# Performance work log

Measured on AMD Instinct MI355X. Metric: run time of the kernel, lower is better.

Reference implementation:

```python
import jax, jax.numpy as jnp
import numpy as np

N = 50000      # nodes
E = 512000     # directed edges (module assumes 2nd half is reverse of 1st half)
DIN = 128      # in_channels
EDIM = 128     # edge_dim (== in_channels, required by HypergraphConv branch)
H = 4          # heads
C = 32         # out_channels per head
EPS = 1e-5     # BatchNorm eps


def _segment_softmax(logits, seg, num):
    # PyG-style scatter softmax over segments (stable: subtract per-segment max)
    m = jax.ops.segment_max(logits, seg, num_segments=num)
    m = jnp.where(jnp.isfinite(m), m, 0.0)
    ex = jnp.exp(logits - m[seg])
    s = jax.ops.segment_sum(ex, seg, num_segments=num)
    return ex / (s[seg] + 1e-16)


def setup_inputs() -> dict:
    key = jax.random.key(0)
    ks = jax.random.split(key, 24)

    def lin(k, fin, fout):
        return (jax.random.normal(k, (fin, fout), jnp.float32) / np.sqrt(fin)).astype(jnp.float32)

    return {
        "x": jax.random.normal(ks[0], (N, DIN), jnp.float32),
        "edge_attr": jax.random.normal(ks[1], (E, EDIM), jnp.float32),
        # TransformerConv params
        "Wq": lin(ks[2], DIN, H * C), "bq": 0.01 * jax.random.normal(ks[3], (H * C,), jnp.float32),
        "Wk": lin(ks[4], DIN, H * C), "bk": 0.01 * jax.random.normal(ks[5], (H * C,), jnp.float32),
        "Wv": lin(ks[6], DIN, H * C), "bv": 0.01 * jax.random.normal(ks[7], (H * C,), jnp.float32),
        "We2": lin(ks[8], EDIM, H * C), "be2": 0.01 * jax.random.normal(ks[9], (H * C,), jnp.float32),
        "We3": lin(ks[10], EDIM, H * C), "be3": 0.01 * jax.random.normal(ks[11], (H * C,), jnp.float32),
        "Wcon": lin(ks[12], H * C, C),
        # BatchNorm1d params
        "bn_w": 1.0 + 0.01 * jax.random.normal(ks[13], (C,), jnp.float32),
        "bn_b": 0.01 * jax.random.normal(ks[14], (C,), jnp.float32),
        # HypergraphConv params (use_attention=False, heads=1)
        "Wh1": lin(ks[15], EDIM, C),
        "Wh2": lin(ks[16], DIN, C),
        "bh": jnp.zeros((C,), jnp.float32),
        # integer inputs
        "edge_index": jax.random.randint(ks[17], (2, E), 0, N, dtype=jnp.int32),
        "batch": jnp.zeros((N,), jnp.int32),
    }


def reference(x, edge_attr, Wq, bq, Wk, bk, Wv, bv, We2, be2, We3, be3, Wcon,
              bn_w, bn_b, Wh1, Wh2, bh, edge_index, batch):
    n = x.shape[0]
    e = edge_index.shape[1]
    src, dst = edge_index[0], edge_index[1]

    # ---- TransformerConv (edge-attention message passing) ----
    q = (x @ Wq + bq).reshape(n, H, C)
    k = (x @ Wk + bk).reshape(n, H, C)
    v = (x @ Wv + bv).reshape(n, H, C)
    ea2 = (edge_attr @ We2 + be2).reshape(e, H, C)
    ea3 = (edge_attr @ We3 + be3).reshape(e, H, C)
    qi, kj, vj = q[dst], k[src], v[src]          # gather per edge: [E,H,C]
    scale = 1.0 / np.sqrt(C)
    a1 = _segment_softmax((qi * kj).sum(-1) * scale, dst, n)    # [E,H]
    a2 = _segment_softmax((qi * ea2).sum(-1) * scale, dst, n)   # [E,H]
    msg = (vj * a1[..., None] + ea3 * a2[..., None]).reshape(e, H * C) @ Wcon  # [E,C]
    x_gat = jax.ops.segment_sum(msg, dst, num_segments=n)       # [N,C]

    # BatchNorm1d (training-mode batch stats, biased var) + exact GELU
    mu = x_gat.mean(0)
    var = ((x_gat - mu) ** 2).mean(0)
    x_gat = jax.nn.gelu(bn_w * (x_gat - mu) * jax.lax.rsqrt(var + EPS) + bn_b,
                        approximate=False)

    # ---- DHT dual hypergraph + HypergraphConv (no attention) ----
    e2 = e // 2
    ei = edge_index[:, :e2]           # first half of (bidirectional) edges
    ea = edge_attr[:e2]
    he_node = jnp.repeat(jnp.arange(e2, dtype=jnp.int32), 2)  # dual-node (edge) ids, [2*E2]
    he_edge = ei.T.reshape(-1)                                 # hyperedge (orig node) ids, [2*E2]

    xh = ea @ Wh1      # lin(edge_attr): [E2,C] (heads=1)
    attr = x @ Wh2     # lin2(x):        [N,C]

    ones = jnp.ones((2 * e2,), jnp.float32)
    deg_d = jax.ops.segment_sum(ones, he_node, num_segments=e2)   # D (== 2 per edge)
    Dinv = jnp.where(deg_d > 0, 1.0 / deg_d, 0.0)
    deg_b = jax.ops.segment_sum(ones, he_edge, num_segments=n)    # B (node degree)
    Binv = jnp.where(deg_b > 0, 1.0 / deg_b, 0.0)

    # propagate 1: dual-node -> hyperedge, norm B, then add hyperedge_attr
    o1 = jax.ops.segment_sum(Binv[he_edge][:, None] * xh[he_node],
                             he_edge, num_segments=n) + attr       # [N,C]
    # propagate 2 (flipped): hyperedge -> dual-node, norm D, add bias
    edge_attr2 = jax.ops.segment_sum(Dinv[he_node][:, None] * o1[he_edge],
                                     he_node, num_segments=e2) + bh  # [E2,C]

    return (x_gat, edge_attr2)
```

## Files before the change

kernel.cpp:

```cpp
#include <hip/hip_runtime.h>
#include <math.h>

#define NN 50000
#define NE 512000
#define NE2 256000
#define SCALE 0.17677669529663687f
#define EPSV 1e-5f
#define CHUNK 128000

#define OFF_Q      0UL
#define OFF_K      6400000UL
#define OFF_V      12800000UL
#define OFF_ATTR   0UL
#define OFF_O1     1600000UL
#define OFF_XGAT   3200000UL
#define OFF_O1ACC  4800000UL
#define OFF_DEGB   6400000UL
#define OFF_STATS  6450000UL
#define OFF_EX1    19200000UL
#define OFF_EX2    21248000UL
#define OFF_CC     23296000UL
#define OFF_S1     31488000UL
#define OFF_S2     31688000UL
#define OFF_XH     19200000UL
#define OFF_AGG    31888000UL
#define OFF_WBT    38288000UL
#define OFF_BIASB  38304384UL

typedef __attribute__((ext_vector_type(8))) short bf16x8;
typedef __attribute__((ext_vector_type(8))) unsigned short us8;
typedef __attribute__((ext_vector_type(4))) float f32x4;

__device__ __forceinline__ unsigned short f2bf(float f) {
    unsigned int u = __float_as_uint(f);
    unsigned int r = (u + 0x7FFFu + ((u >> 16) & 1u)) >> 16;
    return (unsigned short)r;
}
__device__ __forceinline__ float bf2f(unsigned short u) {
    return __uint_as_float(((unsigned int)u) << 16);
}

__global__ void pack_w(const float* __restrict__ We2, const float* __restrict__ be2,
                       const float* __restrict__ We3, const float* __restrict__ be3,
                       unsigned short* __restrict__ WbT, float* __restrict__ biasb) {
    const int idx = blockIdx.x * 256 + threadIdx.x;
    if (idx < 32768) {
        const int j = idx >> 7;
        const int k = idx & 127;
        const float w = (j < 128) ? We2[k * 128 + j] : We3[k * 128 + (j - 128)];
        WbT[idx] = f2bf(w);
    } else if (idx < 33024) {
        const int jj = idx - 32768;
        biasb[jj] = (jj < 128) ? be2[jj] : be3[jj - 128];
    }
}

__global__ __launch_bounds__(256)
void gemm_ea(const float* __restrict__ A, const unsigned short* __restrict__ WbT,
             const float* __restrict__ biasb, unsigned short* __restrict__ Cc, int half) {
    __shared__ unsigned short As[128 * 72];
    __shared__ unsigned short Bs[128 * 72];
    const int tid = threadIdx.x;
    const int wave = tid >> 6;
    const int lane = tid & 63;
    const int quad = lane >> 4;
    const int l16 = lane & 15;
    const int m0 = (wave & 1) * 64;
    const int n0 = (wave >> 1) * 64;
    const size_t r0 = (size_t)blockIdx.x * 128;

    f32x4 acc[4][4];
    #pragma unroll
    for (int i = 0; i < 4; i++)
        #pragma unroll
        for (int j = 0; j < 4; j++) acc[i][j] = (f32x4){0.f, 0.f, 0.f, 0.f};

    for (int kh = 0; kh < 2; kh++) {
        #pragma unroll
        for (int i = 0; i < 8; i++) {
            const int q = tid + 256 * i;
            const int row = q >> 4;
            const int c4 = q & 15;
            const float4 a4 = *(const float4*)(A + (r0 + row) * 128 + kh * 64 + c4 * 4);
            ushort4 b4;
            b4.x = f2bf(a4.x); b4.y = f2bf(a4.y); b4.z = f2bf(a4.z); b4.w = f2bf(a4.w);
            *(ushort4*)(&As[row * 72 + c4 * 4]) = b4;
        }
        {
            const int n = tid >> 1;
            const int koff = (tid & 1) * 32;
            const unsigned short* src = WbT + (size_t)(half * 128 + n) * 128 + kh * 64 + koff;
            #pragma unroll
            for (int u = 0; u < 4; u++) {
                *(us8*)(&Bs[n * 72 + koff + 8 * u]) = *(const us8*)(src + 8 * u);
            }
        }
        __syncthreads();
        #pragma unroll
        for (int kc = 0; kc < 64; kc += 32) {
            bf16x8 af[4], bf[4];
            #pragma unroll
            for (int i = 0; i < 4; i++)
                af[i] = *(const bf16x8*)(&As[(m0 + 16 * i + l16) * 72 + kc + quad * 8]);
            #pragma unroll
            for (int j = 0; j < 4; j++)
                bf[j] = *(const bf16x8*)(&Bs[(n0 + 16 * j + l16) * 72 + kc + quad * 8]);
            #pragma unroll
            for (int i = 0; i < 4; i++)
                #pragma unroll
                for (int j = 0; j < 4; j++)
                    acc[i][j] = __builtin_amdgcn_mfma_f32_16x16x32_bf16(af[i], bf[j], acc[i][j], 0, 0, 0);
        }
        __syncthreads();
    }
    #pragma unroll
    for (int j = 0; j < 4; j++) {
        const int col = n0 + 16 * j + l16;
        const float bcol = biasb[half * 128 + col];
        #pragma unroll
        for (int i = 0; i < 4; i++) {
            #pragma unroll
            for (int r = 0; r < 4; r++) {
                const int row = m0 + 16 * i + quad * 4 + r;
                Cc[(r0 + row) * 128 + col] = f2bf(acc[i][j][r] + bcol);
            }
        }
    }
}

__global__ void qkv_kernel(const float* __restrict__ x,
                           const float* __restrict__ Wq, const float* __restrict__ bq,
                           const float* __restrict__ Wk, const float* __restrict__ bk,
                           const float* __restrict__ Wv, const float* __restrict__ bv,
                           float* __restrict__ q, float* __restrict__ k, float* __restrict__ v) {
    __shared__ float xs[8 * 128];
    const int tid = threadIdx.x;
    const int j = tid & 127;
    const int g = tid >> 7;
    const size_t n0 = (size_t)blockIdx.x * 8;
    ((float4*)xs)[tid] = ((const float4*)(x + n0 * 128))[tid];
    __syncthreads();
    float aq[4] = {0,0,0,0}, ak[4] = {0,0,0,0}, av[4] = {0,0,0,0};
    #pragma unroll 4
    for (int d = 0; d < 128; d++) {
        const float wq = Wq[d*128 + j];
        const float wk = Wk[d*128 + j];
        const float wv = Wv[d*128 + j];
        #pragma unroll
        for (int r = 0; r < 4; r++) {
            const float xv = xs[(g + 2*r)*128 + d];
            aq[r] += xv * wq; ak[r] += xv * wk; av[r] += xv * wv;
        }
    }
    const float bqv = bq[j], bkv = bk[j], bvv = bv[j];
    #pragma unroll
    for (int r = 0; r < 4; r++) {
        const size_t n = n0 + g + 2*r;
        q[n*128 + j] = aq[r] + bqv;
        k[n*128 + j] = ak[r] + bkv;
        v[n*128 + j] = av[r] + bvv;
    }
}

__global__ void pass1(const int* __restrict__ eidx,
                      const float* __restrict__ q, const float* __restrict__ k,
                      const unsigned short* __restrict__ Cc, long e_base,
                      float* __restrict__ ex1, float* __restrict__ ex2,
                      float* __restrict__ s1, float* __restrict__ s2) {
    const size_t e = (size_t)e_base + blockIdx.x * 4 + (threadIdx.x >> 6);
    const int lane = threadIdx.x & 63;
    const int src = eidx[e];
    const int dst = eidx[NE + e];
    const float2 qv = ((const float2*)(q + (size_t)dst * 128))[lane];
    const float2 kv = ((const float2*)(k + (size_t)src * 128))[lane];
    const unsigned int cc = ((const unsigned int*)(Cc + (e - e_base) * 128))[lane];
    const float ea2a = bf2f((unsigned short)(cc & 0xFFFF));
    const float ea2b = bf2f((unsigned short)(cc >> 16));
    float p1 = qv.x * kv.x + qv.y * kv.y;
    float p2 = qv.x * ea2a + qv.y * ea2b;
    #pragma unroll
    for (int off = 8; off > 0; off >>= 1) {
        p1 += __shfl_down(p1, off, 16);
        p2 += __shfl_down(p2, off, 16);
    }
    if ((lane & 15) == 0) {
        const int h = lane >> 4;
        const float v1 = __expf(p1 * SCALE);
        const float v2 = __expf(p2 * SCALE);
        ex1[e * 4 + h] = v1;
        ex2[e * 4 + h] = v2;
        atomicAdd(&s1[(size_t)dst * 4 + h], v1);
        atomicAdd(&s2[(size_t)dst * 4 + h], v2);
    }
}

__global__ void pass2(const int* __restrict__ eidx,
                      const float* __restrict__ v,
                      const unsigned short* __restrict__ Cc, long e_base,
                      const float* __restrict__ ex1, const float* __restrict__ ex2,
                      const float* __restrict__ s1, const float* __restrict__ s2,
                      float* __restrict__ agg) {
    const size_t e = (size_t)e_base + blockIdx.x * 4 + (threadIdx.x >> 6);
    const int lane = threadIdx.x & 63;
    const int src = eidx[e];
    const int dst = eidx[NE + e];
    float a1l = 0.f, a2l = 0.f;
    if (lane < 4) {
        a1l = ex1[e * 4 + lane] / (s1[(size_t)dst * 4 + lane] + 1e-16f);
        a2l = ex2[e * 4 + lane] / (s2[(size_t)dst * 4 + lane] + 1e-16f);
    }
    const int h1 = lane >> 5;
    const int h2 = 2 + (lane >> 5);
    const float a1c1 = __shfl(a1l, h1), a1c2 = __shfl(a1l, h2);
    const float a2c1 = __shfl(a2l, h1), a2c2 = __shfl(a2l, h2);
    const float vv1 = v[(size_t)src * 128 + lane];
    const float vv2 = v[(size_t)src * 128 + lane + 64];
    const float e31 = bf2f(Cc[(e - e_base) * 128 + lane]);
    const float e32 = bf2f(Cc[(e - e_base) * 128 + lane + 64]);
    atomicAdd(&agg[(size_t)dst * 128 + lane],      a1c1 * vv1 + a2c1 * e31);
    atomicAdd(&agg[(size_t)dst * 128 + lane + 64], a1c2 * vv2 + a2c2 * e32);
}

__global__ void gemm_d128_o32(const float* __restrict__ A, const float* __restrict__ W,
                              float* __restrict__ out) {
    __shared__ float as[8 * 128];
    const int tid = threadIdx.x;
    const int p = tid & 31;
    const int mm = tid >> 5;
    const size_t m0 = (size_t)blockIdx.x * 8;
    ((float4*)as)[tid] = ((const float4*)(A + m0 * 128))[tid];
    __syncthreads();
    float c0 = 0.f, c1 = 0.f, c2 = 0.f, c3 = 0.f;
    const float4* as4 = (const float4*)as;
    #pragma unroll 8
    for (int i = 0; i < 32; i++) {
        const float4 a4 = as4[mm*32 + i];
        c0 += a4.x * W[(4*i+0)*32 + p];
        c1 += a4.y * W[(4*i+1)*32 + p];
        c2 += a4.z * W[(4*i+2)*32 + p];
        c3 += a4.w * W[(4*i+3)*32 + p];
    }
    out[(m0 + mm)*32 + p] = (c0 + c1) + (c2 + c3);
}

__global__ void bn_stats(const float* __restrict__ xg, float* __restrict__ stats) {
    __shared__ float ls[256], lss[256];
    const int tid = threadIdx.x;
    float s = 0.f, ss = 0.f;
    for (size_t i = (size_t)blockIdx.x*256 + tid; i < (size_t)NN*32; i += (size_t)gridDim.x*256) {
        const float val = xg[i];
        s += val; ss += val * val;
    }
    ls[tid] = s; lss[tid] = ss;
    __syncthreads();
    if (tid < 32) {
        float as_ = 0.f, ass = 0.f;
        #pragma unroll
        for (int w = 0; w < 8; w++) { as_ += ls[tid + 32*w]; ass += lss[tid + 32*w]; }
        atomicAdd(&stats[tid], as_);
        atomicAdd(&stats[32 + tid], ass);
    }
}

__global__ void bn_gelu(const float* __restrict__ xg, const float* __restrict__ stats,
                        const float* __restrict__ bnw, const float* __restrict__ bnb,
                        float* __restrict__ out) {
    const size_t i = (size_t)blockIdx.x * 256 + threadIdx.x;
    const int c = i & 31;
    const float mu = stats[c] * (1.0f / NN);
    const float var = stats[32 + c] * (1.0f / NN) - mu * mu;
    const float xn = bnw[c] * (xg[i] - mu) * rsqrtf(var + EPSV) + bnb[c];
    out[i] = 0.5f * xn * (1.0f + erff(xn * 0.70710678118654752f));
}

__global__ void hyper_scatter(const float* __restrict__ xh, const int* __restrict__ eidx,
                              float* __restrict__ o1acc, float* __restrict__ degb) {
    const int tid = threadIdx.x;
    const int c = tid & 31;
    const size_t i = (size_t)blockIdx.x * 8 + (tid >> 5);
    const int src = eidx[i];
    const int dst = eidx[NE + i];
    const float xv = xh[i*32 + c];
    atomicAdd(&o1acc[(size_t)src*32 + c], xv);
    atomicAdd(&o1acc[(size_t)dst*32 + c], xv);
    if (c == 0) {
        atomicAdd(&degb[src], 1.0f);
        atomicAdd(&degb[dst], 1.0f);
    }
}

__global__ void o1_finalize(const float* __restrict__ o1acc, const float* __restrict__ degb,
                            const float* __restrict__ attr, float* __restrict__ o1) {
    const size_t i = (size_t)blockIdx.x * 256 + threadIdx.x;
    const int n = (int)(i >> 5);
    const float d = degb[n];
    const float binv = d > 0.f ? 1.0f / d : 0.0f;
    o1[i] = o1acc[i] * binv + attr[i];
}

__global__ void edge_out(const float* __restrict__ o1, const int* __restrict__ eidx,
                         const float* __restrict__ bh, float* __restrict__ out2) {
    const size_t idx = (size_t)blockIdx.x * 256 + threadIdx.x;
    const size_t i = idx >> 5;
    const int c = (int)(idx & 31);
    const int src = eidx[i];
    const int dst = eidx[NE + i];
    out2[idx] = 0.5f * (o1[(size_t)src*32 + c] + o1[(size_t)dst*32 + c]) + bh[c];
}

extern "C" void kernel_launch(void* const* d_in, const int* in_sizes, int n_in,
                              void* d_out, int out_size, void* d_ws, size_t ws_size,
                              hipStream_t stream) {
    const float* x    = (const float*)d_in[0];
    const float* eatt = (const float*)d_in[1];
    const float* Wq   = (const float*)d_in[2];
    const float* bq   = (const float*)d_in[3];
    const float* Wk   = (const float*)d_in[4];
    const float* bk   = (const float*)d_in[5];
    const float* Wv   = (const float*)d_in[6];
    const float* bv   = (const float*)d_in[7];
    const float* We2  = (const float*)d_in[8];
    const float* be2  = (const float*)d_in[9];
    const float* We3  = (const float*)d_in[10];
    const float* be3  = (const float*)d_in[11];
    const float* Wcon = (const float*)d_in[12];
    const float* bnw  = (const float*)d_in[13];
    const float* bnb  = (const float*)d_in[14];
    const float* Wh1  = (const float*)d_in[15];
    const float* Wh2  = (const float*)d_in[16];
    const float* bh   = (const float*)d_in[17];
    const int*   eidx = (const int*)d_in[18];

    float* ws = (float*)d_ws;
    float* q     = ws + OFF_Q;
    float* k     = ws + OFF_K;
    float* v     = ws + OFF_V;
    float* ex1   = ws + OFF_EX1;
    float* ex2   = ws + OFF_EX2;
    unsigned short* Cc = (unsigned short*)(ws + OFF_CC);
    float* s1    = ws + OFF_S1;
    float* s2    = ws + OFF_S2;
    float* agg   = ws + OFF_AGG;
    unsigned short* WbT = (unsigned short*)(ws + OFF_WBT);
    float* biasb = ws + OFF_BIASB;
    float* attr  = ws + OFF_ATTR;
    float* o1    = ws + OFF_O1;
    float* xgat  = ws + OFF_XGAT;
    float* o1acc = ws + OFF_O1ACC;
    float* degb  = ws + OFF_DEGB;
    float* stats = ws + OFF_STATS;
    float* xh    = ws + OFF_XH;
    float* out0  = (float*)d_out;
    float* out1  = (float*)d_out + (size_t)NN * 32;

    hipMemsetAsync(ws + OFF_S1, 0, (38288000UL - OFF_S1) * sizeof(float), stream);

    pack_w<<<129, 256, 0, stream>>>(We2, be2, We3, be3, WbT, biasb);
    qkv_kernel<<<6250, 256, 0, stream>>>(x, Wq, bq, Wk, bk, Wv, bv, q, k, v);

    for (int c = 0; c < 4; c++) {
        const long eb = (long)c * CHUNK;
        gemm_ea<<<1000, 256, 0, stream>>>(eatt + (size_t)eb * 128, WbT, biasb, Cc, 0);
        pass1<<<32000, 256, 0, stream>>>(eidx, q, k, Cc, eb, ex1, ex2, s1, s2);
    }
    for (int c = 0; c < 4; c++) {
        const long eb = (long)c * CHUNK;
        gemm_ea<<<1000, 256, 0, stream>>>(eatt + (size_t)eb * 128, WbT, biasb, Cc, 1);
        pass2<<<32000, 256, 0, stream>>>(eidx, v, Cc, eb, ex1, ex2, s1, s2, agg);
    }

    hipMemsetAsync(ws + OFF_O1ACC, 0, (6450064UL - OFF_O1ACC) * sizeof(float), stream);

    gemm_d128_o32<<<6250, 256, 0, stream>>>(agg, Wcon, xgat);
    bn_stats<<<256, 256, 0, stream>>>(xgat, stats);
    bn_gelu<<<6250, 256, 0, stream>>>(xgat, stats, bnw, bnb, out0);

    gemm_d128_o32<<<32000, 256, 0, stream>>>(eatt, Wh1, xh);
    gemm_d128_o32<<<6250, 256, 0, stream>>>(x, Wh2, attr);
    hyper_scatter<<<32000, 256, 0, stream>>>(xh, eidx, o1acc, degb);
    o1_finalize<<<6250, 256, 0, stream>>>(o1acc, degb, attr, o1);
    edge_out<<<32000, 256, 0, stream>>>(o1, eidx, bh, out1);
}
```

Before: 1.294 ms.

## Fuse edge-attribute GEMM into attention passes via shared-memory staging

```diff
diff --git a/kernel.cpp b/kernel.cpp
--- a/kernel.cpp
+++ b/kernel.cpp
@@ -6,7 +6,6 @@
 #define NE2 256000
 #define SCALE 0.17677669529663687f
 #define EPSV 1e-5f
-#define CHUNK 128000
 
 #define OFF_Q      0UL
 #define OFF_K      6400000UL
@@ -19,7 +18,6 @@
 #define OFF_STATS  6450000UL
 #define OFF_EX1    19200000UL
 #define OFF_EX2    21248000UL
-#define OFF_CC     23296000UL
 #define OFF_S1     31488000UL
 #define OFF_S2     31688000UL
 #define OFF_XH     19200000UL
@@ -30,6 +28,8 @@
 typedef __attribute__((ext_vector_type(8))) short bf16x8;
 typedef __attribute__((ext_vector_type(8))) unsigned short us8;
 typedef __attribute__((ext_vector_type(4))) float f32x4;
+
+#define ESTRIDE 136
 
 __device__ __forceinline__ unsigned short f2bf(float f) {
     unsigned int u = __float_as_uint(f);
@@ -55,19 +55,18 @@
     }
 }
 
-__global__ __launch_bounds__(256)
-void gemm_ea(const float* __restrict__ A, const unsigned short* __restrict__ WbT,
-             const float* __restrict__ biasb, unsigned short* __restrict__ Cc, int half) {
-    __shared__ unsigned short As[128 * 72];
-    __shared__ unsigned short Bs[128 * 72];
-    const int tid = threadIdx.x;
+__device__ __forceinline__ void gemm_tile(const float* __restrict__ A,
+                                          const unsigned short* __restrict__ WbT,
+                                          const float* __restrict__ biasb, const int half,
+                                          unsigned short* sh, const size_t r0, const int tid) {
+    unsigned short* As = sh;
+    unsigned short* Bs = sh + 9216;
     const int wave = tid >> 6;
     const int lane = tid & 63;
     const int quad = lane >> 4;
     const int l16 = lane & 15;
     const int m0 = (wave & 1) * 64;
     const int n0 = (wave >> 1) * 64;
-    const size_t r0 = (size_t)blockIdx.x * 128;
 
     f32x4 acc[4][4];
     #pragma unroll
@@ -122,9 +121,89 @@
             #pragma unroll
             for (int r = 0; r < 4; r++) {
                 const int row = m0 + 16 * i + quad * 4 + r;
-                Cc[(r0 + row) * 128 + col] = f2bf(acc[i][j][r] + bcol);
+                sh[row * ESTRIDE + col] = f2bf(acc[i][j][r] + bcol);
             }
         }
+    }
+    __syncthreads();
+}
+
+__global__ __launch_bounds__(256)
+void gemm_pass1(const float* __restrict__ eatt, const unsigned short* __restrict__ WbT,
+                const float* __restrict__ biasb, const int* __restrict__ eidx,
+                const float* __restrict__ q, const float* __restrict__ k,
+                float* __restrict__ ex1, float* __restrict__ ex2,
+                float* __restrict__ s1, float* __restrict__ s2) {
+    __shared__ unsigned short sh[18432];
+    const int tid = threadIdx.x;
+    const size_t r0 = (size_t)blockIdx.x * 128;
+    gemm_tile(eatt, WbT, biasb, 0, sh, r0, tid);
+
+    const int wave = tid >> 6;
+    const int lane = tid & 63;
+    for (int t = 0; t < 32; t++) {
+        const int lrow = wave * 32 + t;
+        const size_t e = r0 + lrow;
+        const int src = eidx[e];
+        const int dst = eidx[NE + e];
+        const float2 qv = ((const float2*)(q + (size_t)dst * 128))[lane];
+        const float2 kv = ((const float2*)(k + (size_t)src * 128))[lane];
+        const unsigned int cc = *(const unsigned int*)(&sh[lrow * ESTRIDE + lane * 2]);
+        const float ea2a = bf2f((unsigned short)(cc & 0xFFFF));
+        const float ea2b = bf2f((unsigned short)(cc >> 16));
+        float p1 = qv.x * kv.x + qv.y * kv.y;
+        float p2 = qv.x * ea2a + qv.y * ea2b;
+        #pragma unroll
+        for (int off = 8; off > 0; off >>= 1) {
+            p1 += __shfl_down(p1, off, 16);
+            p2 += __shfl_down(p2, off, 16);
+        }
+        if ((lane & 15) == 0) {
+            const int h = lane >> 4;
+            const float v1 = __expf(p1 * SCALE);
+            const float v2 = __expf(p2 * SCALE);
+            ex1[e * 4 + h] = v1;
+            ex2[e * 4 + h] = v2;
+            atomicAdd(&s1[(size_t)dst * 4 + h], v1);
+            atomicAdd(&s2[(size_t)dst * 4 + h], v2);
+        }
+    }
+}
+
+__global__ __launch_bounds__(256)
+void gemm_pass2(const float* __restrict__ eatt, const unsigned short* __restrict__ WbT,
+                const float* __restrict__ biasb, const int* __restrict__ eidx,
+                const float* __restrict__ v,
+                const float* __restrict__ ex1, const float* __restrict__ ex2,
+                const float* __restrict__ s1, const float* __restrict__ s2,
+                float* __restrict__ agg) {
+    __shared__ unsigned short sh[18432];
+    const int tid = threadIdx.x;
+    const size_t r0 = (size_t)blockIdx.x * 128;
+    gemm_tile(eatt, WbT, biasb, 1, sh, r0, tid);
+
+    const int wave = tid >> 6;
+    const int lane = tid & 63;
+    for (int t = 0; t < 32; t++) {
+        const int lrow = wave * 32 + t;
+        const size_t e = r0 + lrow;
+        const int src = eidx[e];
+        const int dst = eidx[NE + e];
+        float a1l = 0.f, a2l = 0.f;
+        if (lane < 4) {
+            a1l = ex1[e * 4 + lane] / (s1[(size_t)dst * 4 + lane] + 1e-16f);
+            a2l = ex2[e * 4 + lane] / (s2[(size_t)dst * 4 + lane] + 1e-16f);
+        }
+        const int h1 = lane >> 5;
+        const int h2 = 2 + (lane >> 5);
+        const float a1c1 = __shfl(a1l, h1), a1c2 = __shfl(a1l, h2);
+        const float a2c1 = __shfl(a2l, h1), a2c2 = __shfl(a2l, h2);
+        const float vv1 = v[(size_t)src * 128 + lane];
+        const float vv2 = v[(size_t)src * 128 + lane + 64];
+        const float e31 = bf2f(sh[lrow * ESTRIDE + lane]);
+        const float e32 = bf2f(sh[lrow * ESTRIDE + lane + 64]);
+        atomicAdd(&agg[(size_t)dst * 128 + lane],      a1c1 * vv1 + a2c1 * e31);
+        atomicAdd(&agg[(size_t)dst * 128 + lane + 64], a1c2 * vv2 + a2c2 * e32);
     }
 }
 
@@ -160,65 +239,6 @@
         k[n*128 + j] = ak[r] + bkv;
         v[n*128 + j] = av[r] + bvv;
     }
-}
-
-__global__ void pass1(const int* __restrict__ eidx,
-                      const float* __restrict__ q, const float* __restrict__ k,
-                      const unsigned short* __restrict__ Cc, long e_base,
-                      float* __restrict__ ex1, float* __restrict__ ex2,
-                      float* __restrict__ s1, float* __restrict__ s2) {
-    const size_t e = (size_t)e_base + blockIdx.x * 4 + (threadIdx.x >> 6);
-    const int lane = threadIdx.x & 63;
-    const int src = eidx[e];
-    const int dst = eidx[NE + e];
-    const float2 qv = ((const float2*)(q + (size_t)dst * 128))[lane];
-    const float2 kv = ((const float2*)(k + (size_t)src * 128))[lane];
-    const unsigned int cc = ((const unsigned int*)(Cc + (e - e_base) * 128))[lane];
-    const float ea2a = bf2f((unsigned short)(cc & 0xFFFF));
-    const float ea2b = bf2f((unsigned short)(cc >> 16));
-    float p1 = qv.x * kv.x + qv.y * kv.y;
-    float p2 = qv.x * ea2a + qv.y * ea2b;
-    #pragma unroll
-    for (int off = 8; off > 0; off >>= 1) {
-        p1 += __shfl_down(p1, off, 16);
-        p2 += __shfl_down(p2, off, 16);
-    }
-    if ((lane & 15) == 0) {
-        const int h = lane >> 4;
-        const float v1 = __expf(p1 * SCALE);
-        const float v2 = __expf(p2 * SCALE);
-        ex1[e * 4 + h] = v1;
-        ex2[e * 4 + h] = v2;
-        atomicAdd(&s1[(size_t)dst * 4 + h], v1);
-        atomicAdd(&s2[(size_t)dst * 4 + h], v2);
-    }
-}
-
-__global__ void pass2(const int* __restrict__ eidx,
-                      const float* __restrict__ v,
-                      const unsigned short* __restrict__ Cc, long e_base,
-                      const float* __restrict__ ex1, const float* __restrict__ ex2,
-                      const float* __restrict__ s1, const float* __restrict__ s2,
-                      float* __restrict__ agg) {
-    const size_t e = (size_t)e_base + blockIdx.x * 4 + (threadIdx.x >> 6);
-    const int lane = threadIdx.x & 63;
-    const int src = eidx[e];
-    const int dst = eidx[NE + e];
-    float a1l = 0.f, a2l = 0.f;
-    if (lane < 4) {
-        a1l = ex1[e * 4 + lane] / (s1[(size_t)dst * 4 + lane] + 1e-16f);
-        a2l = ex2[e * 4 + lane] / (s2[(size_t)dst * 4 + lane] + 1e-16f);
-    }
-    const int h1 = lane >> 5;
-    const int h2 = 2 + (lane >> 5);
-    const float a1c1 = __shfl(a1l, h1), a1c2 = __shfl(a1l, h2);
-    const float a2c1 = __shfl(a2l, h1), a2c2 = __shfl(a2l, h2);
-    const float vv1 = v[(size_t)src * 128 + lane];
-    const float vv2 = v[(size_t)src * 128 + lane + 64];
-    const float e31 = bf2f(Cc[(e - e_base) * 128 + lane]);
-    const float e32 = bf2f(Cc[(e - e_base) * 128 + lane + 64]);
-    atomicAdd(&agg[(size_t)dst * 128 + lane],      a1c1 * vv1 + a2c1 * e31);
-    atomicAdd(&agg[(size_t)dst * 128 + lane + 64], a1c2 * vv2 + a2c2 * e32);
 }
 
 __global__ void gemm_d128_o32(const float* __restrict__ A, const float* __restrict__ W,
@@ -337,7 +357,6 @@
     float* v     = ws + OFF_V;
     float* ex1   = ws + OFF_EX1;
     float* ex2   = ws + OFF_EX2;
-    unsigned short* Cc = (unsigned short*)(ws + OFF_CC);
     float* s1    = ws + OFF_S1;
     float* s2    = ws + OFF_S2;
     float* agg   = ws + OFF_AGG;
@@ -358,16 +377,8 @@
     pack_w<<<129, 256, 0, stream>>>(We2, be2, We3, be3, WbT, biasb);
     qkv_kernel<<<6250, 256, 0, stream>>>(x, Wq, bq, Wk, bk, Wv, bv, q, k, v);
 
-    for (int c = 0; c < 4; c++) {
-        const long eb = (long)c * CHUNK;
-        gemm_ea<<<1000, 256, 0, stream>>>(eatt + (size_t)eb * 128, WbT, biasb, Cc, 0);
-        pass1<<<32000, 256, 0, stream>>>(eidx, q, k, Cc, eb, ex1, ex2, s1, s2);
-    }
-    for (int c = 0; c < 4; c++) {
-        const long eb = (long)c * CHUNK;
-        gemm_ea<<<1000, 256, 0, stream>>>(eatt + (size_t)eb * 128, WbT, biasb, Cc, 1);
-        pass2<<<32000, 256, 0, stream>>>(eidx, v, Cc, eb, ex1, ex2, s1, s2, agg);
-    }
+    gemm_pass1<<<4000, 256, 0, stream>>>(eatt, WbT, biasb, eidx, q, k, ex1, ex2, s1, s2);
+    gemm_pass2<<<4000, 256, 0, stream>>>(eatt, WbT, biasb, eidx, v, ex1, ex2, s1, s2, agg);
 
     hipMemsetAsync(ws + OFF_O1ACC, 0, (6450064UL - OFF_O1ACC) * sizeof(float), stream);
 
```

Result: slower. 1.404 ms (+8.5%).

## Sort edges by destination (CSR) and fuse attention passes without atomics

Applied to the files above, without the earlier changes.

```diff
diff --git a/kernel.cpp b/kernel.cpp
--- a/kernel.cpp
+++ b/kernel.cpp
@@ -6,7 +6,6 @@
 #define NE2 256000
 #define SCALE 0.17677669529663687f
 #define EPSV 1e-5f
-#define CHUNK 128000
 
 #define OFF_Q      0UL
 #define OFF_K      6400000UL
@@ -19,13 +18,18 @@
 #define OFF_STATS  6450000UL
 #define OFF_EX1    19200000UL
 #define OFF_EX2    21248000UL
-#define OFF_CC     23296000UL
-#define OFF_S1     31488000UL
-#define OFF_S2     31688000UL
 #define OFF_XH     19200000UL
-#define OFF_AGG    31888000UL
-#define OFF_WBT    38288000UL
-#define OFF_BIASB  38304384UL
+#define OFF_CC2    23296000UL
+#define OFF_CC3    56064000UL
+#define OFF_SEG    88832000UL
+#define OFF_CUR    88883000UL
+#define OFF_CNT    88933000UL
+#define OFF_INV    88983000UL
+#define OFF_SRCS   89495000UL
+#define OFF_PART   90007000UL
+#define OFF_WBT    90008000UL
+#define OFF_BIASB  90024384UL
+#define OFF_AGG    90024640UL
 
 typedef __attribute__((ext_vector_type(8))) short bf16x8;
 typedef __attribute__((ext_vector_type(8))) unsigned short us8;
@@ -55,9 +59,64 @@
     }
 }
 
+__global__ void k_hist(const int* __restrict__ eidx, int* __restrict__ cnt) {
+    const int e = blockIdx.x * 256 + threadIdx.x;
+    atomicAdd(&cnt[eidx[NE + e]], 1);
+}
+
+__global__ void k_scanA(const int* __restrict__ cnt, int* __restrict__ seg,
+                        int* __restrict__ part) {
+    __shared__ int sd[256];
+    const int tid = threadIdx.x;
+    const int i = blockIdx.x * 256 + tid;
+    const int v = (i < NN) ? cnt[i] : 0;
+    sd[tid] = v;
+    __syncthreads();
+    for (int off = 1; off < 256; off <<= 1) {
+        int t = (tid >= off) ? sd[tid - off] : 0;
+        __syncthreads();
+        sd[tid] += t;
+        __syncthreads();
+    }
+    if (i < NN) seg[i] = sd[tid] - v;
+    if (tid == 255) part[blockIdx.x] = sd[255];
+}
+
+__global__ void k_scanB(int* __restrict__ part) {
+    __shared__ int sd[256];
+    const int tid = threadIdx.x;
+    const int v = (tid < 196) ? part[tid] : 0;
+    sd[tid] = v;
+    __syncthreads();
+    for (int off = 1; off < 256; off <<= 1) {
+        int t = (tid >= off) ? sd[tid - off] : 0;
+        __syncthreads();
+        sd[tid] += t;
+        __syncthreads();
+    }
+    if (tid < 196) part[tid] = sd[tid] - v;
+}
+
+__global__ void k_scanC(int* __restrict__ seg, const int* __restrict__ part) {
+    const int i = blockIdx.x * 256 + threadIdx.x;
+    if (i < NN) seg[i] += part[blockIdx.x];
+    if (i == 0) seg[NN] = NE;
+}
+
+__global__ void k_scatter(const int* __restrict__ eidx, const int* __restrict__ seg,
+                          int* __restrict__ cur, int* __restrict__ inv,
+                          int* __restrict__ srcs) {
+    const int e = blockIdx.x * 256 + threadIdx.x;
+    const int dst = eidx[NE + e];
+    const int pos = seg[dst] + atomicAdd(&cur[dst], 1);
+    inv[e] = pos;
+    srcs[pos] = eidx[e];
+}
+
 __global__ __launch_bounds__(256)
 void gemm_ea(const float* __restrict__ A, const unsigned short* __restrict__ WbT,
-             const float* __restrict__ biasb, unsigned short* __restrict__ Cc, int half) {
+             const float* __restrict__ biasb, const int* __restrict__ inv,
+             unsigned short* __restrict__ Cc, int half) {
     __shared__ unsigned short As[128 * 72];
     __shared__ unsigned short Bs[128 * 72];
     const int tid = threadIdx.x;
@@ -113,6 +172,12 @@
         }
         __syncthreads();
     }
+    int posr[16];
+    #pragma unroll
+    for (int i = 0; i < 4; i++)
+        #pragma unroll
+        for (int r = 0; r < 4; r++)
+            posr[i * 4 + r] = inv[r0 + m0 + 16 * i + quad * 4 + r];
     #pragma unroll
     for (int j = 0; j < 4; j++) {
         const int col = n0 + 16 * j + l16;
@@ -121,8 +186,7 @@
         for (int i = 0; i < 4; i++) {
             #pragma unroll
             for (int r = 0; r < 4; r++) {
-                const int row = m0 + 16 * i + quad * 4 + r;
-                Cc[(r0 + row) * 128 + col] = f2bf(acc[i][j][r] + bcol);
+                Cc[(size_t)posr[i * 4 + r] * 128 + col] = f2bf(acc[i][j][r] + bcol);
             }
         }
     }
@@ -162,63 +226,56 @@
     }
 }
 
-__global__ void pass1(const int* __restrict__ eidx,
-                      const float* __restrict__ q, const float* __restrict__ k,
-                      const unsigned short* __restrict__ Cc, long e_base,
-                      float* __restrict__ ex1, float* __restrict__ ex2,
-                      float* __restrict__ s1, float* __restrict__ s2) {
-    const size_t e = (size_t)e_base + blockIdx.x * 4 + (threadIdx.x >> 6);
+__global__ __launch_bounds__(256)
+void attn_pass(const int* __restrict__ seg, const int* __restrict__ srcs,
+               const float* __restrict__ q, const float* __restrict__ k,
+               const float* __restrict__ v,
+               const unsigned short* __restrict__ Cc2, const unsigned short* __restrict__ Cc3,
+               float* __restrict__ ex1, float* __restrict__ ex2,
+               float* __restrict__ agg) {
     const int lane = threadIdx.x & 63;
-    const int src = eidx[e];
-    const int dst = eidx[NE + e];
-    const float2 qv = ((const float2*)(q + (size_t)dst * 128))[lane];
-    const float2 kv = ((const float2*)(k + (size_t)src * 128))[lane];
-    const unsigned int cc = ((const unsigned int*)(Cc + (e - e_base) * 128))[lane];
-    const float ea2a = bf2f((unsigned short)(cc & 0xFFFF));
-    const float ea2b = bf2f((unsigned short)(cc >> 16));
-    float p1 = qv.x * kv.x + qv.y * kv.y;
-    float p2 = qv.x * ea2a + qv.y * ea2b;
-    #pragma unroll
-    for (int off = 8; off > 0; off >>= 1) {
-        p1 += __shfl_down(p1, off, 16);
-        p2 += __shfl_down(p2, off, 16);
-    }
-    if ((lane & 15) == 0) {
-        const int h = lane >> 4;
-        const float v1 = __expf(p1 * SCALE);
-        const float v2 = __expf(p2 * SCALE);
-        ex1[e * 4 + h] = v1;
-        ex2[e * 4 + h] = v2;
-        atomicAdd(&s1[(size_t)dst * 4 + h], v1);
-        atomicAdd(&s2[(size_t)dst * 4 + h], v2);
-    }
-}
-
-__global__ void pass2(const int* __restrict__ eidx,
-                      const float* __restrict__ v,
-                      const unsigned short* __restrict__ Cc, long e_base,
-                      const float* __restrict__ ex1, const float* __restrict__ ex2,
-                      const float* __restrict__ s1, const float* __restrict__ s2,
-                      float* __restrict__ agg) {
-    const size_t e = (size_t)e_base + blockIdx.x * 4 + (threadIdx.x >> 6);
-    const int lane = threadIdx.x & 63;
-    const int src = eidx[e];
-    const int dst = eidx[NE + e];
-    float a1l = 0.f, a2l = 0.f;
-    if (lane < 4) {
-        a1l = ex1[e * 4 + lane] / (s1[(size_t)dst * 4 + lane] + 1e-16f);
-        a2l = ex2[e * 4 + lane] / (s2[(size_t)dst * 4 + lane] + 1e-16f);
-    }
-    const int h1 = lane >> 5;
-    const int h2 = 2 + (lane >> 5);
-    const float a1c1 = __shfl(a1l, h1), a1c2 = __shfl(a1l, h2);
-    const float a2c1 = __shfl(a2l, h1), a2c2 = __shfl(a2l, h2);
-    const float vv1 = v[(size_t)src * 128 + lane];
-    const float vv2 = v[(size_t)src * 128 + lane + 64];
-    const float e31 = bf2f(Cc[(e - e_base) * 128 + lane]);
-    const float e32 = bf2f(Cc[(e - e_base) * 128 + lane + 64]);
-    atomicAdd(&agg[(size_t)dst * 128 + lane],      a1c1 * vv1 + a2c1 * e31);
-    atomicAdd(&agg[(size_t)dst * 128 + lane + 64], a1c2 * vv2 + a2c2 * e32);
+    const int d = blockIdx.x * 4 + (threadIdx.x >> 6);
+    const int s0 = seg[d], s1 = seg[d + 1];
+    const float2 qv = ((const float2*)(q + (size_t)d * 128))[lane];
+    const int h = lane >> 4;
+
+    float sh1 = 0.f, sh2 = 0.f;
+    for (int i = s0; i < s1; i++) {
+        const int src = srcs[i];
+        const float2 kv = ((const float2*)(k + (size_t)src * 128))[lane];
+        const unsigned int cc = ((const unsigned int*)Cc2)[(size_t)i * 64 + lane];
+        float p1 = qv.x * kv.x + qv.y * kv.y;
+        float p2 = qv.x * bf2f((unsigned short)(cc & 0xFFFF))
+                 + qv.y * bf2f((unsigned short)(cc >> 16));
+        #pragma unroll
+        for (int off = 8; off > 0; off >>= 1) {
+            p1 += __shfl_down(p1, off, 16);
+            p2 += __shfl_down(p2, off, 16);
+        }
+        if ((lane & 15) == 0) {
+            const float v1 = __expf(p1 * SCALE);
+            const float v2 = __expf(p2 * SCALE);
+            ex1[(size_t)i * 4 + h] = v1;
+            ex2[(size_t)i * 4 + h] = v2;
+            sh1 += v1; sh2 += v2;
+        }
+    }
+    const float r1 = 1.f / (sh1 + 1e-16f);
+    const float r2 = 1.f / (sh2 + 1e-16f);
+    const float i1 = __shfl(r1, h * 16);
+    const float i2 = __shfl(r2, h * 16);
+
+    float ax = 0.f, ay = 0.f;
+    for (int i = s0; i < s1; i++) {
+        const int src = srcs[i];
+        const float2 vv = ((const float2*)(v + (size_t)src * 128))[lane];
+        const unsigned int c3 = ((const unsigned int*)Cc3)[(size_t)i * 64 + lane];
+        const float a1 = ex1[(size_t)i * 4 + h] * i1;
+        const float a2 = ex2[(size_t)i * 4 + h] * i2;
+        ax += a1 * vv.x + a2 * bf2f((unsigned short)(c3 & 0xFFFF));
+        ay += a1 * vv.y + a2 * bf2f((unsigned short)(c3 >> 16));
+    }
+    ((float2*)(agg + (size_t)d * 128))[lane] = (float2){ax, ay};
 }
 
 __global__ void gemm_d128_o32(const float* __restrict__ A, const float* __restrict__ W,
@@ -337,12 +394,17 @@
     float* v     = ws + OFF_V;
     float* ex1   = ws + OFF_EX1;
     float* ex2   = ws + OFF_EX2;
-    unsigned short* Cc = (unsigned short*)(ws + OFF_CC);
-    float* s1    = ws + OFF_S1;
-    float* s2    = ws + OFF_S2;
-    float* agg   = ws + OFF_AGG;
+    unsigned short* Cc2 = (unsigned short*)(ws + OFF_CC2);
+    unsigned short* Cc3 = (unsigned short*)(ws + OFF_CC3);
+    int* seg  = (int*)(ws + OFF_SEG);
+    int* cur  = (int*)(ws + OFF_CUR);
+    int* cnt  = (int*)(ws + OFF_CNT);
+    int* inv  = (int*)(ws + OFF_INV);
+    int* srcs = (int*)(ws + OFF_SRCS);
+    int* part = (int*)(ws + OFF_PART);
     unsigned short* WbT = (unsigned short*)(ws + OFF_WBT);
     float* biasb = ws + OFF_BIASB;
+    float* agg   = ws + OFF_AGG;
     float* attr  = ws + OFF_ATTR;
     float* o1    = ws + OFF_O1;
     float* xgat  = ws + OFF_XGAT;
@@ -353,21 +415,22 @@
     float* out0  = (float*)d_out;
     float* out1  = (float*)d_out + (size_t)NN * 32;
 
-    hipMemsetAsync(ws + OFF_S1, 0, (38288000UL - OFF_S1) * sizeof(float), stream);
+    hipMemsetAsync(ws + OFF_CUR, 0, 100000 * sizeof(int), stream);
 
     pack_w<<<129, 256, 0, stream>>>(We2, be2, We3, be3, WbT, biasb);
+
+    k_hist<<<2000, 256, 0, stream>>>(eidx, cnt);
+    k_scanA<<<196, 256, 0, stream>>>(cnt, seg, part);
+    k_scanB<<<1, 256, 0, stream>>>(part);
+    k_scanC<<<196, 256, 0, stream>>>(seg, part);
+    k_scatter<<<2000, 256, 0, stream>>>(eidx, seg, cur, inv, srcs);
+
     qkv_kernel<<<6250, 256, 0, stream>>>(x, Wq, bq, Wk, bk, Wv, bv, q, k, v);
 
-    for (int c = 0; c < 4; c++) {
-        const long eb = (long)c * CHUNK;
-        gemm_ea<<<1000, 256, 0, stream>>>(eatt + (size_t)eb * 128, WbT, biasb, Cc, 0);
-        pass1<<<32000, 256, 0, stream>>>(eidx, q, k, Cc, eb, ex1, ex2, s1, s2);
-    }
-    for (int c = 0; c < 4; c++) {
-        const long eb = (long)c * CHUNK;
-        gemm_ea<<<1000, 256, 0, stream>>>(eatt + (size_t)eb * 128, WbT, biasb, Cc, 1);
-        pass2<<<32000, 256, 0, stream>>>(eidx, v, Cc, eb, ex1, ex2, s1, s2, agg);
-    }
+    gemm_ea<<<4000, 256, 0, stream>>>(eatt, WbT, biasb, inv, Cc2, 0);
+    gemm_ea<<<4000, 256, 0, stream>>>(eatt, WbT, biasb, inv, Cc3, 1);
+
+    attn_pass<<<12500, 256, 0, stream>>>(seg, srcs, q, k, v, Cc2, Cc3, ex1, ex2, agg);
 
     hipMemsetAsync(ws + OFF_O1ACC, 0, (6450064UL - OFF_O1ACC) * sizeof(float), stream);
 
```

New measurement: 1.180 ms. -8.8%, faster.
